# Kernel optimization log

Hardware: AMD Instinct MI355X
Metric: run time of the kernel (lower is better)

## Reference

```python
import jax, jax.numpy as jnp
import numpy as np

H = 1024     # hidden_size
NH = 16      # num heads
HD = H // NH # head_dim = 64
I = 4096     # intermediate_size
EPS = 1e-6


def rmsnorm(x, w, eps=EPS):
    var = jnp.mean(jnp.square(x), axis=-1, keepdims=True)
    return x * jax.lax.rsqrt(var + eps) * w


def attention(x, ctx, wq, wk, wv, wo):
    # x: [B,S,H], ctx: [B,Skv,H]; weights stored [in,out]
    B, S, _ = x.shape
    Skv = ctx.shape[1]
    q = (x @ wq).reshape(B, S, NH, HD)
    k = (ctx @ wk).reshape(B, Skv, NH, HD)
    v = (ctx @ wv).reshape(B, Skv, NH, HD)
    scores = jnp.einsum('bqhd,bkhd->bhqk', q, k) * (HD ** -0.5)
    attn = jax.nn.softmax(scores.astype(jnp.float32), axis=-1).astype(q.dtype)
    out = jnp.einsum('bhqk,bkhd->bqhd', attn, v).reshape(B, S, NH * HD)
    return out @ wo


def mlp(x, wg, wu, wd):
    return (jax.nn.silu(x @ wg) * (x @ wu)) @ wd


def setup_inputs() -> dict:
    key = jax.random.key(0)
    ks = jax.random.split(key, 16)
    p = lambda k, shape: (jax.random.normal(k, shape, jnp.float32) * 0.02)
    return {
        'hidden_states': jax.random.normal(ks[0], (1, 2048, H), jnp.float32),
        'context': jax.random.normal(ks[1], (1, 2048, H), jnp.float32),
        'sa_norm_w': jnp.ones((H,), jnp.float32),
        'sa_wq': p(ks[2], (H, NH * HD)),
        'sa_wk': p(ks[3], (H, NH * HD)),
        'sa_wv': p(ks[4], (H, NH * HD)),
        'sa_wo': p(ks[5], (NH * HD, H)),
        'ca_norm_w': jnp.ones((H,), jnp.float32),
        'ca_wq': p(ks[6], (H, NH * HD)),
        'ca_wk': p(ks[7], (H, NH * HD)),
        'ca_wv': p(ks[8], (H, NH * HD)),
        'ca_wo': p(ks[9], (NH * HD, H)),
        'mlp_norm_w': jnp.ones((H,), jnp.float32),
        'w_gate': p(ks[10], (H, I)),
        'w_up': p(ks[11], (H, I)),
        'w_down': p(ks[12], (I, H)),
    }


def reference(hidden_states, context, sa_norm_w, sa_wq, sa_wk, sa_wv, sa_wo,
              ca_norm_w, ca_wq, ca_wk, ca_wv, ca_wo,
              mlp_norm_w, w_gate, w_up, w_down):
    # self-attention block
    residual = hidden_states
    h = rmsnorm(hidden_states, sa_norm_w)
    h = residual + attention(h, h, sa_wq, sa_wk, sa_wv, sa_wo)
    # cross-attention block
    residual = h
    hn = rmsnorm(h, ca_norm_w)
    h = residual + attention(hn, context, ca_wq, ca_wk, ca_wv, ca_wo)
    # MLP block
    residual = h
    hn = rmsnorm(h, mlp_norm_w)
    h = residual + mlp(hn, w_gate, w_up, w_down)
    return h
```

## Files before the change

### kernel.cpp

```cpp
#include <hip/hip_runtime.h>

#define H 1024
#define S 2048
#define NH 16
#define HD 64
#define ISZ 4096

typedef __attribute__((ext_vector_type(8))) short s8v;
typedef __attribute__((ext_vector_type(4))) short s4v;
typedef __attribute__((ext_vector_type(4))) float f4v;
typedef __attribute__((ext_vector_type(2))) unsigned u2v;

#define MFMA16 __builtin_amdgcn_mfma_f32_16x16x32_bf16

__device__ __forceinline__ short f2bf(float f) {
    unsigned u = __builtin_bit_cast(unsigned, f);
    unsigned r = (u + 0x7FFFu + ((u >> 16) & 1u)) >> 16;
    return (short)r;
}
__device__ __forceinline__ float bf2f(short s) {
    unsigned u = ((unsigned)(unsigned short)s) << 16;
    return __builtin_bit_cast(float, u);
}
__device__ __forceinline__ float exp2_hw(float x) {
    float r; asm("v_exp_f32 %0, %1" : "=v"(r) : "v"(x)); return r;
}
__device__ __forceinline__ unsigned cvt_pk_bf16(float lo, float hi) {
    unsigned r; asm("v_cvt_pk_bf16_f32 %0, %1, %2" : "=v"(r) : "v"(lo), "v"(hi)); return r;
}

__device__ __forceinline__ void gload_lds16(const short* g, short* l) {
    __builtin_amdgcn_global_load_lds(
        (const __attribute__((address_space(1))) void*)g,
        (__attribute__((address_space(3))) void*)l, 16, 0, 0);
}

template <int N> struct VMt { static constexpr int val = N; };

struct PreArgs {
    const void* hid; const void* ctx;
    const void* sanw; const void* canw; const void* mlpnw;
    const void* w[11];
    short* hidc; short* ctxc; short* xn;
    short* canw_o; short* mlpnw_o;
    short* wT[11];
    int* flag_out;
};

__device__ __forceinline__ void tr_tile(const void* src, short* dst, int K, int N,
                                        int k0, int n0, int rmul, int roff,
                                        int isbf, float* tile ) {
    int t = threadIdx.x;
    int c = t & 31, r0 = t >> 5;
    if (isbf) {
        const short* s = (const short*)src;
#pragma unroll
        for (int i = 0; i < 4; i++)
            tile[(r0 + i * 8) * 33 + c] = bf2f(s[(k0 + r0 + i * 8) * N + n0 + c]);
    } else {
        const float* s = (const float*)src;
#pragma unroll
        for (int i = 0; i < 4; i++)
            tile[(r0 + i * 8) * 33 + c] = s[(k0 + r0 + i * 8) * N + n0 + c];
    }
    __syncthreads();
#pragma unroll
    for (int i = 0; i < 4; i++)
        dst[((n0 + r0 + i * 8) * rmul + roff) * K + k0 + c] = f2bf(tile[c * 33 + r0 + i * 8]);
}

__global__ __launch_bounds__(256) void preamble_kernel(PreArgs pa) {
    __shared__ float tile[32 * 33];
    __shared__ float red[4];
    int b = blockIdx.x;
    int t = threadIdx.x;
    int isbf = (((const unsigned*)pa.sanw)[0] == 0x3F803F80u);
    if (blockIdx.x == 0 && t == 0) pa.flag_out[0] = isbf;

    if (b < 2048) {
        int row = b;
        float xf[4];
        if (isbf) {
            s4v xv = *(const s4v*)((const short*)pa.hid + row * H + t * 4);
#pragma unroll
            for (int j = 0; j < 4; j++) xf[j] = bf2f(xv[j]);
        } else {
            const float* s = (const float*)pa.hid + row * H + t * 4;
#pragma unroll
            for (int j = 0; j < 4; j++) xf[j] = s[j];
        }
        float ss = 0.f;
        s4v cv;
#pragma unroll
        for (int j = 0; j < 4; j++) { cv[j] = f2bf(xf[j]); xf[j] = bf2f(cv[j]); ss += xf[j] * xf[j]; }
        *(s4v*)(pa.hidc + row * H + t * 4) = cv;
        int lane = t & 63, wid = t >> 6;
#pragma unroll
        for (int off = 32; off >= 1; off >>= 1) ss += __shfl_xor(ss, off);
        if (lane == 0) red[wid] = ss;
        __syncthreads();
        float tot = red[0] + red[1] + red[2] + red[3];
        float scale = rsqrtf(tot * (1.f / (float)H) + 1e-6f);
        float wv[4];
        if (isbf) {
            s4v wq = *(const s4v*)((const short*)pa.sanw + t * 4);
#pragma unroll
            for (int j = 0; j < 4; j++) wv[j] = bf2f(wq[j]);
        } else {
            const float* s = (const float*)pa.sanw + t * 4;
#pragma unroll
            for (int j = 0; j < 4; j++) wv[j] = s[j];
        }
        s4v ov;
#pragma unroll
        for (int j = 0; j < 4; j++) ov[j] = f2bf(xf[j] * scale * wv[j]);
        *(s4v*)(pa.xn + row * H + t * 4) = ov;
        return;
    }
    b -= 2048;
    if (b < 1024) {
        int i8 = b * 2048 + t * 8;
        if (isbf) {
            *(s8v*)(pa.ctxc + i8) = *(const s8v*)((const short*)pa.ctx + i8);
        } else {
            const float* s = (const float*)pa.ctx;
            s8v o;
#pragma unroll
            for (int j = 0; j < 8; j++) o[j] = f2bf(s[i8 + j]);
            *(s8v*)(pa.ctxc + i8) = o;
        }
        return;
    }
    b -= 1024;
    if (b < 2) {
        const void* src = (b == 0) ? pa.canw : pa.mlpnw;
        short* dst = (b == 0) ? pa.canw_o : pa.mlpnw_o;
        if (isbf) { if (t * 4 < H) *(s4v*)(dst + t * 4) = *(const s4v*)((const short*)src + t * 4); }
        else {
            const float* s = (const float*)src;
            s4v o;
#pragma unroll
            for (int j = 0; j < 4; j++) o[j] = f2bf(s[t * 4 + j]);
            *(s4v*)(dst + t * 4) = o;
        }
        return;
    }
    b -= 2;
    if (b < 8 * 1024) {
        int w = b >> 10, tl = b & 1023;
        tr_tile(pa.w[w], pa.wT[w], H, H, (tl & 31) * 32, (tl >> 5) * 32, 1, 0, isbf, tile);
        return;
    }
    b -= 8 * 1024;
    if (b < 2 * 4096) {
        int w = 8 + (b >> 12), tl = b & 4095;
        tr_tile(pa.w[w], pa.wT[8], H, ISZ, (tl & 31) * 32, (tl >> 5) * 32, 2, w - 8, isbf, tile);
        return;
    }
    b -= 2 * 4096;
    {
        tr_tile(pa.w[10], pa.wT[10], ISZ, H, (b & 127) * 32, (b >> 7) * 32, 1, 0, isbf, tile);
    }
}

__global__ __launch_bounds__(256) void rmsnorm_kernel(const short* __restrict__ x,
                                                      const short* __restrict__ w,
                                                      short* __restrict__ out) {
    int row = blockIdx.x;
    int t = threadIdx.x;
    int lane = t & 63, wid = t >> 6;
    const short* xr = x + row * H;

    s4v xv = *(const s4v*)(xr + t * 4);
    float xf[4];
    float ss = 0.f;
#pragma unroll
    for (int j = 0; j < 4; j++) { xf[j] = bf2f(xv[j]); ss += xf[j] * xf[j]; }
#pragma unroll
    for (int off = 32; off >= 1; off >>= 1) ss += __shfl_xor(ss, off);

    __shared__ float red[4];
    if (lane == 0) red[wid] = ss;
    __syncthreads();
    float tot = red[0] + red[1] + red[2] + red[3];
    float scale = rsqrtf(tot * (1.f / (float)H) + 1e-6f);

    s4v wv = *(const s4v*)(w + t * 4);
    s4v ov;
#pragma unroll
    for (int j = 0; j < 4; j++) ov[j] = f2bf(xf[j] * scale * bf2f(wv[j]));
    *(s4v*)(out + row * H + t * 4) = ov;
}

template <int BM_, int BN_>
__global__ __launch_bounds__(512, 2) void gemm_bt_kernel(
    const short* __restrict__ A0, const short* __restrict__ A1, int split, int lda,
    const short* __restrict__ Bt,
    void* __restrict__ C, int ldc, int K,
    const short* __restrict__ res,
    const int* __restrict__ dtype_flag,
    short* __restrict__ vtbuf, int vcol0,
    short* __restrict__ silu_out) {

    constexpr int MC = BM_ / 32;
    constexpr int NC = BN_ / 64;
    constexpr int U  = (BM_ + BN_) / 8;
    constexpr int PT = U / 8;
    constexpr int BUF = (BM_ + BN_) * 64;

    __shared__ short lds[2 * BUF];

    const short* A = (blockIdx.y < split) ? A0 : A1;
    int m0 = blockIdx.x * BM_;
    int n0 = blockIdx.y * BN_;

    int t = threadIdx.x;
    int lane = t & 63, wid = t >> 6;
    int quad = lane >> 4, l15 = lane & 15;
    int wr = wid >> 2, wc = wid & 3;
    int ld4 = lane >> 2, lc8 = (lane & 3) * 8;

    f4v acc[MC][NC] = {};

    auto stage = [&](short* buf, int k0) {
#pragma unroll
        for (int s = 0; s < PT; ++s) {
            int u = wid * PT + s;
            if (u < BM_ / 8) {
                int h = u / (BM_ / 16), r16 = u % (BM_ / 16);
                gload_lds16(A + (m0 + r16 * 16 + ld4) * lda + k0 + h * 32 + lc8,
                            buf + h * (BM_ * 32) + r16 * 512);
            } else {
                int ub = u - BM_ / 8;
                int h = ub / (BN_ / 16), r16 = ub % (BN_ / 16);
                gload_lds16(Bt + (n0 + r16 * 16 + ld4) * K + k0 + h * 32 + lc8,
                            buf + BM_ * 64 + h * (BN_ * 32) + r16 * 512);
            }
        }
    };

    auto compute = [&](const short* buf) {
#pragma unroll
        for (int kh = 0; kh < 2; ++kh) {
            s8v af[MC], bfv[NC];
#pragma unroll
            for (int mc = 0; mc < MC; ++mc)
                af[mc] = *(const s8v*)(buf + kh * (BM_ * 32) +
                                       (wr * (BM_ / 2) + mc * 16 + l15) * 32 + quad * 8);
#pragma unroll
            for (int nc = 0; nc < NC; ++nc)
                bfv[nc] = *(const s8v*)(buf + BM_ * 64 + kh * (BN_ * 32) +
                                        (wc * (BN_ / 4) + nc * 16 + l15) * 32 + quad * 8);
#pragma unroll
            for (int mc = 0; mc < MC; ++mc)
#pragma unroll
                for (int nc = 0; nc < NC; ++nc)
                    acc[mc][nc] = MFMA16(af[mc], bfv[nc], acc[mc][nc], 0, 0, 0);
        }
    };

    const int KT = K / 64;
    stage(lds, 0);
    __syncthreads();
    int cur = 0;
    for (int kt = 0; kt < KT - 1; ++kt) {
        stage(lds + (cur ^ 1) * BUF, (kt + 1) * 64);
        compute(lds + cur * BUF);
        __syncthreads();
        cur ^= 1;
    }
    compute(lds + cur * BUF);

    if (silu_out) {
#pragma unroll
        for (int mc = 0; mc < MC; mc++) {
#pragma unroll
            for (int nc = 0; nc < NC; nc++) {
                int row = m0 + wr * (BM_ / 2) + mc * 16 + quad * 4;
                int col = n0 + wc * (BN_ / 4) + nc * 16 + l15;
#pragma unroll
                for (int r = 0; r < 4; r++) {
                    float v = acc[mc][nc][r];
                    float other = __shfl_xor(v, 1);
                    if ((l15 & 1) == 0) {
                        float sig = 1.f / (1.f + __expf(-v));
                        silu_out[(row + r) * ISZ + (col >> 1)] = f2bf(v * sig * other);
                    }
                }
            }
        }
        return;
    }

    int out_fp32 = (dtype_flag != nullptr) && (dtype_flag[0] == 0);

#pragma unroll
    for (int mc = 0; mc < MC; mc++) {
#pragma unroll
        for (int nc = 0; nc < NC; nc++) {
            int row = m0 + wr * (BM_ / 2) + mc * 16 + quad * 4;
            int col = n0 + wc * (BN_ / 4) + nc * 16 + l15;
#pragma unroll
            for (int r = 0; r < 4; r++) {
                float vf = acc[mc][nc][r];
                if (res) vf += bf2f(res[(row + r) * ldc + col]);
                if (vtbuf && col >= vcol0)
                    vtbuf[(col - vcol0) * S + row + r] = f2bf(vf);
                else if (out_fp32)
                    ((float*)C)[(row + r) * ldc + col] = vf;
                else
                    ((short*)C)[(row + r) * ldc + col] = f2bf(vf);
            }
        }
    }
}

template <int BM_, int BN_>
__global__ __launch_bounds__(512, 2) void gemm_np_kernel(
    const short* __restrict__ A, int lda,
    const short* __restrict__ Bt,
    void* __restrict__ C, int ldc, int K,
    const short* __restrict__ res,
    const int* __restrict__ dtype_flag) {

    constexpr int MC = BM_ / 32;
    constexpr int NC = BN_ / 64;
    constexpr int PT = (BM_ + BN_) / 64;
    constexpr int BUF = (BM_ + BN_) * 64;

    __shared__ short lds[4 * BUF];

    int lin = blockIdx.x;
    int sw = (lin & 7) * 32 + (lin >> 3);
    int m0 = (sw & 31) * BM_;
    int n0 = (sw >> 5) * BN_;

    int t_ = threadIdx.x;
    int lane = t_ & 63, wid = t_ >> 6;
    int quad = lane >> 4, l15 = lane & 15;
    int wr = wid >> 2, wc = wid & 3;
    int ld4 = lane >> 2;
    int lcs = (((lane & 3) ^ ((ld4 >> 1) & 3)) * 8);
    int sq  = quad ^ ((l15 >> 1) & 3);

    f4v acc[MC][NC] = {};

    auto stage = [&](int bi, int kt) {
        short* buf = lds + bi * BUF;
        int k0 = kt * 64;
#pragma unroll
        for (int s = 0; s < PT; ++s) {
            int u = wid * PT + s;
            if (u < BM_ / 8) {
                int hh = u / (BM_ / 16), r16 = u % (BM_ / 16);
                gload_lds16(A + (m0 + r16 * 16 + ld4) * lda + k0 + hh * 32 + lcs,
                            buf + hh * (BM_ * 32) + r16 * 512);
            } else {
                int ub = u - BM_ / 8;
                int hh = ub / (BN_ / 16), r16 = ub % (BN_ / 16);
                gload_lds16(Bt + (n0 + r16 * 16 + ld4) * K + k0 + hh * 32 + lcs,
                            buf + BM_ * 64 + hh * (BN_ * 32) + r16 * 512);
            }
        }
    };

    auto tile = [&](int t, auto wt) {
        constexpr int W = decltype(wt)::val;
        if constexpr (W == 9)      asm volatile("s_waitcnt vmcnt(9)" ::: "memory");
        else if constexpr (W == 6) asm volatile("s_waitcnt vmcnt(6)" ::: "memory");
        else if constexpr (W == 3) asm volatile("s_waitcnt vmcnt(3)" ::: "memory");
        else                       asm volatile("s_waitcnt vmcnt(0)" ::: "memory");
        __builtin_amdgcn_s_barrier();
        const short* bc = lds + (t & 3) * BUF;
        s8v af[2][MC], bv[2][NC];
#pragma unroll
        for (int kh = 0; kh < 2; ++kh) {
#pragma unroll
            for (int mc = 0; mc < MC; ++mc)
                af[kh][mc] = *(const s8v*)(bc + kh * (BM_ * 32) +
                                           (wr * (BM_ / 2) + mc * 16 + l15) * 32 + sq * 8);
#pragma unroll
            for (int nc = 0; nc < NC; ++nc)
                bv[kh][nc] = *(const s8v*)(bc + BM_ * 64 + kh * (BN_ * 32) +
                                           (wc * (BN_ / 4) + nc * 16 + l15) * 32 + sq * 8);
        }
        asm volatile("s_waitcnt lgkmcnt(0)" ::: "memory");
        __builtin_amdgcn_s_barrier();
        __builtin_amdgcn_s_setprio(1);
#pragma unroll
        for (int kh = 0; kh < 2; ++kh)
#pragma unroll
            for (int mc = 0; mc < MC; ++mc)
#pragma unroll
                for (int nc = 0; nc < NC; ++nc)
                    acc[mc][nc] = MFMA16(af[kh][mc], bv[kh][nc], acc[mc][nc], 0, 0, 0);
        __builtin_amdgcn_s_setprio(0);
    };

    const int KT = K / 64;
    stage(0, 0); stage(1, 1); stage(2, 2);
    for (int t = 0; t < KT - 3; ++t) {
        stage((t + 3) & 3, t + 3);
        tile(t, VMt<9>{});
    }
    tile(KT - 3, VMt<6>{});
    tile(KT - 2, VMt<3>{});
    tile(KT - 1, VMt<0>{});

    int out_fp32 = (dtype_flag != nullptr) && (dtype_flag[0] == 0);
#pragma unroll
    for (int mc = 0; mc < MC; mc++) {
#pragma unroll
        for (int nc = 0; nc < NC; nc++) {
            int row = m0 + wr * (BM_ / 2) + mc * 16 + quad * 4;
            int col = n0 + wc * (BN_ / 4) + nc * 16 + l15;
#pragma unroll
            for (int r = 0; r < 4; r++) {
                float vf = acc[mc][nc][r];
                if (res) vf += bf2f(res[(row + r) * ldc + col]);
                if (out_fp32)
                    ((float*)C)[(row + r) * ldc + col] = vf;
                else
                    ((short*)C)[(row + r) * ldc + col] = f2bf(vf);
            }
        }
    }
}

__global__ __launch_bounds__(512, 2) void gemm_gu8_kernel(
    const short* __restrict__ A, const short* __restrict__ Bt,
    short* __restrict__ silu_out) {

    __shared__ short lds[65536];

    int lin = blockIdx.x;
    int sw = (lin & 7) * 32 + (lin >> 3);
    int m0 = (sw & 7) * 256;
    int n0 = (sw >> 3) * 256;

    int t = threadIdx.x;
    int lane = t & 63, wid = t >> 6;
    int quad = lane >> 4, l15 = lane & 15;
    int wr = wid >> 2, wc = wid & 3;
    int ld4 = lane >> 2;
    int lcs = (((lane & 3) ^ ((ld4 >> 1) & 3)) * 8);
    int sq  = quad ^ ((l15 >> 1) & 3);

    f4v acc[8][4] = {};

    const short* Arow = A + (m0 + ld4) * 1024 + lcs;
    const short* Brow = Bt + (n0 + ld4) * 1024 + lcs;

    auto stA = [&](int buf, int kt, int kh) {
        short* d = lds + buf * 32768 + kh * 8192;
#pragma unroll
        for (int i = 0; i < 2; i++) {
            int r0 = (wid + 8 * i) * 16;
            gload_lds16(Arow + r0 * 1024 + kt * 64 + kh * 32, d + r0 * 32);
        }
    };
    auto stB = [&](int buf, int kt, int kh) {
        short* d = lds + buf * 32768 + 16384 + kh * 8192;
#pragma unroll
        for (int i = 0; i < 2; i++) {
            int r0 = (wid + 8 * i) * 16;
            gload_lds16(Brow + r0 * 1024 + kt * 64 + kh * 32, d + r0 * 32);
        }
    };

    const int aoff = (wr * 128 + l15) * 32 + sq * 8;
    const int boff = 16384 + (wc * 64 + l15) * 32 + sq * 8;

    stA(0, 0, 0); stB(0, 0, 0); stA(0, 0, 1); stB(0, 0, 1);
    asm volatile("s_waitcnt vmcnt(4)" ::: "memory");
    __builtin_amdgcn_s_barrier();

    int cur = 0;
    for (int kt = 0; kt < 15; ++kt) {
        const short* bc = lds + cur * 32768;
        int nb = cur ^ 1;
        s8v af[8], b0, b1;

#pragma unroll
        for (int mc = 0; mc < 8; ++mc) af[mc] = *(const s8v*)(bc + aoff + mc * 512);
        b0 = *(const s8v*)(bc + boff);
        b1 = *(const s8v*)(bc + boff + 512);
        stA(nb, kt + 1, 0);
        __builtin_amdgcn_s_barrier();
        asm volatile("s_waitcnt lgkmcnt(0)" ::: "memory");
        __builtin_amdgcn_s_setprio(1);
#pragma unroll
        for (int mc = 0; mc < 8; ++mc) {
            acc[mc][0] = MFMA16(af[mc], b0, acc[mc][0], 0, 0, 0);
            acc[mc][1] = MFMA16(af[mc], b1, acc[mc][1], 0, 0, 0);
        }
        __builtin_amdgcn_s_setprio(0);
        __builtin_amdgcn_s_barrier();

        b0 = *(const s8v*)(bc + boff + 1024);
        b1 = *(const s8v*)(bc + boff + 1536);
        stB(nb, kt + 1, 0);
        asm volatile("s_waitcnt vmcnt(4)" ::: "memory");
        __builtin_amdgcn_s_barrier();
        asm volatile("s_waitcnt lgkmcnt(0)" ::: "memory");
        __builtin_amdgcn_s_setprio(1);
#pragma unroll
        for (int mc = 0; mc < 8; ++mc) {
            acc[mc][2] = MFMA16(af[mc], b0, acc[mc][2], 0, 0, 0);
            acc[mc][3] = MFMA16(af[mc], b1, acc[mc][3], 0, 0, 0);
        }
        __builtin_amdgcn_s_setprio(0);
        __builtin_amdgcn_s_barrier();

#pragma unroll
        for (int mc = 0; mc < 8; ++mc) af[mc] = *(const s8v*)(bc + 8192 + aoff + mc * 512);
        b0 = *(const s8v*)(bc + 8192 + boff);
        b1 = *(const s8v*)(bc + 8192 + boff + 512);
        stA(nb, kt + 1, 1);
        __builtin_amdgcn_s_barrier();
        asm volatile("s_waitcnt lgkmcnt(0)" ::: "memory");
        __builtin_amdgcn_s_setprio(1);
#pragma unroll
        for (int mc = 0; mc < 8; ++mc) {
            acc[mc][0] = MFMA16(af[mc], b0, acc[mc][0], 0, 0, 0);
            acc[mc][1] = MFMA16(af[mc], b1, acc[mc][1], 0, 0, 0);
        }
        __builtin_amdgcn_s_setprio(0);
        __builtin_amdgcn_s_barrier();

        b0 = *(const s8v*)(bc + 8192 + boff + 1024);
        b1 = *(const s8v*)(bc + 8192 + boff + 1536);
        stB(nb, kt + 1, 1);
        asm volatile("s_waitcnt vmcnt(4)" ::: "memory");
        __builtin_amdgcn_s_barrier();
        asm volatile("s_waitcnt lgkmcnt(0)" ::: "memory");
        __builtin_amdgcn_s_setprio(1);
#pragma unroll
        for (int mc = 0; mc < 8; ++mc) {
            acc[mc][2] = MFMA16(af[mc], b0, acc[mc][2], 0, 0, 0);
            acc[mc][3] = MFMA16(af[mc], b1, acc[mc][3], 0, 0, 0);
        }
        __builtin_amdgcn_s_setprio(0);
        __builtin_amdgcn_s_barrier();

        cur ^= 1;
    }

    asm volatile("s_waitcnt vmcnt(0)" ::: "memory");
    __builtin_amdgcn_s_barrier();
    {
        const short* bc = lds + cur * 32768;
#pragma unroll
        for (int kh = 0; kh < 2; ++kh) {
            s8v af[8], bv[4];
#pragma unroll
            for (int mc = 0; mc < 8; ++mc) af[mc] = *(const s8v*)(bc + kh * 8192 + aoff + mc * 512);
#pragma unroll
            for (int nc = 0; nc < 4; ++nc) bv[nc] = *(const s8v*)(bc + kh * 8192 + boff + nc * 512);
#pragma unroll
            for (int mc = 0; mc < 8; ++mc)
#pragma unroll
                for (int nc = 0; nc < 4; ++nc)
                    acc[mc][nc] = MFMA16(af[mc], bv[nc], acc[mc][nc], 0, 0, 0);
        }
    }

#pragma unroll
    for (int mc = 0; mc < 8; mc++) {
#pragma unroll
        for (int nc = 0; nc < 4; nc++) {
            int row = m0 + wr * 128 + mc * 16 + quad * 4;
            int col = n0 + wc * 64 + nc * 16 + l15;
#pragma unroll
            for (int r = 0; r < 4; r++) {
                float v = acc[mc][nc][r];
                float other = __shfl_xor(v, 1);
                if ((l15 & 1) == 0) {
                    float sig = 1.f / (1.f + __expf(-v));
                    silu_out[(row + r) * ISZ + (col >> 1)] = f2bf(v * sig * other);
                }
            }
        }
    }
}

__global__ __launch_bounds__(512, 4) void flash_attn_kernel(const short* __restrict__ q,
                                                            const short* __restrict__ kk,
                                                            const short* __restrict__ vt,
                                                            int rs,
                                                            short* __restrict__ o) {
    __shared__ short lds[40960];

    int h = blockIdx.y;
    int q0 = blockIdx.x * 64;
    int t = threadIdx.x;
    int lane = t & 63, wid = t >> 6;
    int quad = lane >> 4, l15 = lane & 15;
    int gw = wid & 3, gh = wid >> 2;
    int kvbase = gh * 1024;
    int kro = l15 & 7;

    int lrow = lane >> 3;
    int lsrc = ((lane & 7) ^ lrow) * 8;

    auto stageKV = [&](int buf, int tt) {
        int kvt = kvbase + tt * 64;
        short* kb = lds + (gh * 2 + buf) * 4096;
        short* vb = lds + 16384 + (gh * 2 + buf) * 4096;
#pragma unroll
        for (int i = 0; i < 2; i++) {
            int r0 = gw * 16 + i * 8;
            gload_lds16(kk + (kvt + r0 + lrow) * rs + h * HD + lsrc, kb + r0 * 64);
            gload_lds16(vt + (h * HD + r0 + lrow) * S + kvt + lsrc, vb + r0 * 64);
        }
    };

    const float qscale = 0.125f * 1.44269504f;
    s8v bq[2];
    int qrow = q0 + gw * 16 + l15;
#pragma unroll
    for (int c = 0; c < 2; c++) {
        s8v raw = *(const s8v*)(q + qrow * rs + h * HD + c * 32 + quad * 8);
#pragma unroll
        for (int j = 0; j < 8; j++) bq[c][j] = f2bf(qscale * bf2f(raw[j]));
    }

    f4v o_acc[4] = {};
    float m_s = -INFINITY, l_s = 0.f;
    short* pw = lds + 32768 + wid * 1024;

    const int NT = 16;
    stageKV(0, 0);
    __syncthreads();
    int cur = 0;
    for (int tt = 0; tt < NT; ++tt) {
        if (tt + 1 < NT) stageKV(cur ^ 1, tt + 1);
        const short* kb = lds + (gh * 2 + cur) * 4096;
        const short* vb = lds + 16384 + (gh * 2 + cur) * 4096;

        f4v st[4];
#pragma unroll
        for (int kc = 0; kc < 4; kc++) {
            f4v a_ = (f4v){0.f, 0.f, 0.f, 0.f};
#pragma unroll
            for (int dc = 0; dc < 2; dc++) {
                s8v kf = *(const s8v*)(kb + (kc * 16 + l15) * 64 + ((dc * 4 + quad) ^ kro) * 8);
                a_ = MFMA16(kf, bq[dc], a_, 0, 0, 0);
            }
            st[kc] = a_;
        }

        float mloc = -INFINITY;
#pragma unroll
        for (int kc = 0; kc < 4; kc++)
#pragma unroll
            for (int r = 0; r < 4; r++) mloc = fmaxf(mloc, st[kc][r]);
        mloc = fmaxf(mloc, __shfl_xor(mloc, 16));
        mloc = fmaxf(mloc, __shfl_xor(mloc, 32));
        float m_new = fmaxf(m_s, mloc);
        float alpha = exp2_hw(m_s - m_new);
        float lloc = 0.f;
#pragma unroll
        for (int kc = 0; kc < 4; kc++)
#pragma unroll
            for (int r = 0; r < 4; r++) {
                float p = exp2_hw(st[kc][r] - m_new);
                st[kc][r] = p;
                lloc += p;
            }
        lloc += __shfl_xor(lloc, 16);
        lloc += __shfl_xor(lloc, 32);
        l_s = l_s * alpha + lloc;
        m_s = m_new;
#pragma unroll
        for (int nd = 0; nd < 4; nd++)
#pragma unroll
            for (int r = 0; r < 4; r++) o_acc[nd][r] *= alpha;

#pragma unroll
        for (int kc = 0; kc < 4; kc++) {
            u2v w;
            w[0] = cvt_pk_bf16(st[kc][0], st[kc][1]);
            w[1] = cvt_pk_bf16(st[kc][2], st[kc][3]);
            int pslot = (kc * 2 + (quad >> 1)) ^ kro;
            *(u2v*)(pw + l15 * 64 + pslot * 8 + (quad & 1) * 4) = w;
        }

#pragma unroll
        for (int nd = 0; nd < 4; nd++) {
#pragma unroll
            for (int kc2 = 0; kc2 < 2; kc2++) {
                s8v vf = *(const s8v*)(vb + (nd * 16 + l15) * 64 + ((kc2 * 4 + quad) ^ kro) * 8);
                s8v pf = *(const s8v*)(pw + l15 * 64 + ((kc2 * 4 + quad) ^ kro) * 8);
                o_acc[nd] = MFMA16(vf, pf, o_acc[nd], 0, 0, 0);
            }
        }
        __syncthreads();
        cur ^= 1;
    }

    float* ex = (float*)lds;
    if (gh == 1) {
        int base = (gw * 64 + lane) * 20;
#pragma unroll
        for (int nd = 0; nd < 4; nd++) *(f4v*)(ex + base + nd * 4) = o_acc[nd];
        ex[base + 16] = m_s;
        ex[base + 17] = l_s;
    }
    __syncthreads();
    if (gh == 1) return;

    int base = (wid * 64 + lane) * 20;
    float mB = ex[base + 16], lB = ex[base + 17];
    float M = fmaxf(m_s, mB);
    float a = exp2_hw(m_s - M), bsc = exp2_hw(mB - M);
    float inv = 1.f / (a * l_s + bsc * lB);
#pragma unroll
    for (int nd = 0; nd < 4; nd++) {
        f4v ob = *(const f4v*)(ex + base + nd * 4);
#pragma unroll
        for (int r = 0; r < 4; r++)
            o_acc[nd][r] = (a * o_acc[nd][r] + bsc * ob[r]) * inv;
    }

#pragma unroll
    for (int nd = 0; nd < 4; nd++)
#pragma unroll
        for (int r = 0; r < 4; r++)
            pw[l15 * 64 + nd * 16 + quad * 4 + r] = f2bf(o_acc[nd][r]);

    int qr = lane >> 2, dc2 = (lane & 3) * 16;
    s8v x0 = *(const s8v*)(pw + qr * 64 + dc2);
    s8v x1 = *(const s8v*)(pw + qr * 64 + dc2 + 8);
    short* dst = o + (q0 + wid * 16 + qr) * H + h * HD + dc2;
    *(s8v*)(dst) = x0;
    *(s8v*)(dst + 8) = x1;
}

extern "C" void kernel_launch(void* const* d_in, const int* in_sizes, int n_in,
                              void* d_out, int out_size, void* d_ws, size_t ws_size,
                              hipStream_t stream) {
    const int SH = S * H;
    const int WH = H * H;
    const int WI = H * ISZ;

    int* flag = (int*)d_ws;
    short* base = (short*)d_ws + 16;

    short* hidc   = base;
    short* ctxc   = hidc + SH;
    short* sanw   = ctxc + SH;
    short* canw   = sanw + H;
    short* mlpnw  = canw + H;
    short* saqkvT = mlpnw + H;
    short* sawoT  = saqkvT + 3 * WH;
    short* caqkvT = sawoT + WH;
    short* cawoT  = caqkvT + 3 * WH;
    short* wguT   = cawoT + WH;
    short* wdT    = wguT + 2 * WI;
    short* xn     = wdT + WI;
    short* qkv    = xn + SH;
    short* ao     = qkv + 3 * SH;
    short* h1     = ao + SH;
    short* gu     = qkv;
    short* h2     = qkv + 8 * SH;
    short* vt     = h2 + SH;

    dim3 blk(256);
    dim3 blk2(512);

    PreArgs pa;
    pa.hid = d_in[0]; pa.ctx = d_in[1];
    pa.sanw = d_in[2]; pa.canw = d_in[7]; pa.mlpnw = d_in[12];
    const void* wsrc[11] = {d_in[3], d_in[4], d_in[5], d_in[6],
                            d_in[8], d_in[9], d_in[10], d_in[11],
                            d_in[13], d_in[14], d_in[15]};
    short* wdst[11] = {saqkvT, saqkvT + WH, saqkvT + 2 * WH, sawoT,
                       caqkvT, caqkvT + WH, caqkvT + 2 * WH, cawoT,
                       wguT, wguT , wdT};
    for (int i = 0; i < 11; i++) { pa.w[i] = wsrc[i]; pa.wT[i] = wdst[i]; }
    pa.hidc = hidc; pa.ctxc = ctxc; pa.xn = xn;
    pa.canw_o = canw; pa.mlpnw_o = mlpnw;
    pa.flag_out = flag;
    const int pre_blocks = 2048 + 1024 + 2 + 8 * 1024 + 2 * 4096 + 4096;
    preamble_kernel<<<pre_blocks, blk, 0, stream>>>(pa);

    gemm_bt_kernel<128, 128><<<dim3(S / 128, 3 * H / 128), blk2, 0, stream>>>(
        xn, xn, 24, H, saqkvT, qkv, 3 * H, H, nullptr, nullptr, vt, 2 * H, nullptr);
    flash_attn_kernel<<<dim3(S / 64, NH), blk2, 0, stream>>>(qkv, qkv + H, vt, 3 * H, ao);
    gemm_np_kernel<64, 128><<<dim3(256), blk2, 0, stream>>>(
        ao, H, sawoT, h1, H, H, hidc, nullptr);

    rmsnorm_kernel<<<S, blk, 0, stream>>>(h1, canw, xn);
    gemm_bt_kernel<128, 128><<<dim3(S / 128, 3 * H / 128), blk2, 0, stream>>>(
        xn, ctxc, 8, H, caqkvT, qkv, 3 * H, H, nullptr, nullptr, vt, 2 * H, nullptr);
    flash_attn_kernel<<<dim3(S / 64, NH), blk2, 0, stream>>>(qkv, qkv + H, vt, 3 * H, ao);
    gemm_np_kernel<64, 128><<<dim3(256), blk2, 0, stream>>>(
        ao, H, cawoT, h2, H, H, h1, nullptr);

    rmsnorm_kernel<<<S, blk, 0, stream>>>(h2, mlpnw, xn);
    gemm_gu8_kernel<<<dim3(256), blk2, 0, stream>>>(xn, wguT, gu);
    gemm_np_kernel<64, 128><<<dim3(256), blk2, 0, stream>>>(
        gu, ISZ, wdT, d_out, H, ISZ, h2, flag);
}
```

Before: 424.5 us.

## Deepen gate/up GEMM pipeline to 4-slot ring with 3 tiles in flight

Restructures the fused gate/up GEMM main loop from double-buffered 64-wide K tiles to a 4-deep ring of 32-wide K tiles. Three tiles are prefetched ahead, with vmcnt waits tuned per tail iteration. The goal is to hide global-to-LDS load latency better. It also removes the XOR swizzle on LDS addressing, which may introduce bank conflicts on the fragment reads.

```diff
diff --git a/kernel.cpp b/kernel.cpp
--- a/kernel.cpp
+++ b/kernel.cpp
@@ -442,50 +442,48 @@
     int lane = t & 63, wid = t >> 6;
     int quad = lane >> 4, l15 = lane & 15;
     int wr = wid >> 2, wc = wid & 3;
-    int ld4 = lane >> 2;
-    int lcs = (((lane & 3) ^ ((ld4 >> 1) & 3)) * 8);
-    int sq  = quad ^ ((l15 >> 1) & 3);
+    int ld4 = lane >> 2, lc8 = (lane & 3) * 8;
 
     f4v acc[8][4] = {};
 
-    const short* Arow = A + (m0 + ld4) * 1024 + lcs;
-    const short* Brow = Bt + (n0 + ld4) * 1024 + lcs;
-
-    auto stA = [&](int buf, int kt, int kh) {
-        short* d = lds + buf * 32768 + kh * 8192;
+    const short* Arow = A + (m0 + ld4) * 1024 + lc8;
+    const short* Brow = Bt + (n0 + ld4) * 1024 + lc8;
+
+    auto stA = [&](int buf, int kt) {
+        short* d = lds + buf * 16384;
 #pragma unroll
         for (int i = 0; i < 2; i++) {
             int r0 = (wid + 8 * i) * 16;
-            gload_lds16(Arow + r0 * 1024 + kt * 64 + kh * 32, d + r0 * 32);
+            gload_lds16(Arow + r0 * 1024 + kt * 32, d + r0 * 32);
         }
     };
-    auto stB = [&](int buf, int kt, int kh) {
-        short* d = lds + buf * 32768 + 16384 + kh * 8192;
+    auto stB = [&](int buf, int kt) {
+        short* d = lds + buf * 16384 + 8192;
 #pragma unroll
         for (int i = 0; i < 2; i++) {
             int r0 = (wid + 8 * i) * 16;
-            gload_lds16(Brow + r0 * 1024 + kt * 64 + kh * 32, d + r0 * 32);
+            gload_lds16(Brow + r0 * 1024 + kt * 32, d + r0 * 32);
         }
     };
 
-    const int aoff = (wr * 128 + l15) * 32 + sq * 8;
-    const int boff = 16384 + (wc * 64 + l15) * 32 + sq * 8;
-
-    stA(0, 0, 0); stB(0, 0, 0); stA(0, 0, 1); stB(0, 0, 1);
-    asm volatile("s_waitcnt vmcnt(4)" ::: "memory");
+    const int aoff = (wr * 128 + l15) * 32 + quad * 8;
+    const int boff = 8192 + (wc * 64 + l15) * 32 + quad * 8;
+
+    stA(0, 0); stB(0, 0);
+    stA(1, 1); stB(1, 1);
+    stA(2, 2); stB(2, 2);
+    asm volatile("s_waitcnt vmcnt(8)" ::: "memory");
     __builtin_amdgcn_s_barrier();
 
-    int cur = 0;
-    for (int kt = 0; kt < 15; ++kt) {
-        const short* bc = lds + cur * 32768;
-        int nb = cur ^ 1;
+    auto ktile = [&](int kt, bool do_stage, auto wt) {
+        constexpr int W = decltype(wt)::val;
+        const short* bc = lds + (kt & 3) * 16384;
         s8v af[8], b0, b1;
-
 #pragma unroll
         for (int mc = 0; mc < 8; ++mc) af[mc] = *(const s8v*)(bc + aoff + mc * 512);
         b0 = *(const s8v*)(bc + boff);
         b1 = *(const s8v*)(bc + boff + 512);
-        stA(nb, kt + 1, 0);
+        if (do_stage) stA((kt + 3) & 3, kt + 3);
         __builtin_amdgcn_s_barrier();
         asm volatile("s_waitcnt lgkmcnt(0)" ::: "memory");
         __builtin_amdgcn_s_setprio(1);
@@ -496,11 +494,12 @@
         }
         __builtin_amdgcn_s_setprio(0);
         __builtin_amdgcn_s_barrier();
-
         b0 = *(const s8v*)(bc + boff + 1024);
         b1 = *(const s8v*)(bc + boff + 1536);
-        stB(nb, kt + 1, 0);
-        asm volatile("s_waitcnt vmcnt(4)" ::: "memory");
+        if (do_stage) stB((kt + 3) & 3, kt + 3);
+        if constexpr (W == 8)      asm volatile("s_waitcnt vmcnt(8)" ::: "memory");
+        else if constexpr (W == 4) asm volatile("s_waitcnt vmcnt(4)" ::: "memory");
+        else if constexpr (W == 0) asm volatile("s_waitcnt vmcnt(0)" ::: "memory");
         __builtin_amdgcn_s_barrier();
         asm volatile("s_waitcnt lgkmcnt(0)" ::: "memory");
         __builtin_amdgcn_s_setprio(1);
@@ -511,59 +510,12 @@
         }
         __builtin_amdgcn_s_setprio(0);
         __builtin_amdgcn_s_barrier();
-
-#pragma unroll
-        for (int mc = 0; mc < 8; ++mc) af[mc] = *(const s8v*)(bc + 8192 + aoff + mc * 512);
-        b0 = *(const s8v*)(bc + 8192 + boff);
-        b1 = *(const s8v*)(bc + 8192 + boff + 512);
-        stA(nb, kt + 1, 1);
-        __builtin_amdgcn_s_barrier();
-        asm volatile("s_waitcnt lgkmcnt(0)" ::: "memory");
-        __builtin_amdgcn_s_setprio(1);
-#pragma unroll
-        for (int mc = 0; mc < 8; ++mc) {
-            acc[mc][0] = MFMA16(af[mc], b0, acc[mc][0], 0, 0, 0);
-            acc[mc][1] = MFMA16(af[mc], b1, acc[mc][1], 0, 0, 0);
-        }
-        __builtin_amdgcn_s_setprio(0);
-        __builtin_amdgcn_s_barrier();
-
-        b0 = *(const s8v*)(bc + 8192 + boff + 1024);
-        b1 = *(const s8v*)(bc + 8192 + boff + 1536);
-        stB(nb, kt + 1, 1);
-        asm volatile("s_waitcnt vmcnt(4)" ::: "memory");
-        __builtin_amdgcn_s_barrier();
-        asm volatile("s_waitcnt lgkmcnt(0)" ::: "memory");
-        __builtin_amdgcn_s_setprio(1);
-#pragma unroll
-        for (int mc = 0; mc < 8; ++mc) {
-            acc[mc][2] = MFMA16(af[mc], b0, acc[mc][2], 0, 0, 0);
-            acc[mc][3] = MFMA16(af[mc], b1, acc[mc][3], 0, 0, 0);
-        }
-        __builtin_amdgcn_s_setprio(0);
-        __builtin_amdgcn_s_barrier();
-
-        cur ^= 1;
-    }
-
-    asm volatile("s_waitcnt vmcnt(0)" ::: "memory");
-    __builtin_amdgcn_s_barrier();
-    {
-        const short* bc = lds + cur * 32768;
-#pragma unroll
-        for (int kh = 0; kh < 2; ++kh) {
-            s8v af[8], bv[4];
-#pragma unroll
-            for (int mc = 0; mc < 8; ++mc) af[mc] = *(const s8v*)(bc + kh * 8192 + aoff + mc * 512);
-#pragma unroll
-            for (int nc = 0; nc < 4; ++nc) bv[nc] = *(const s8v*)(bc + kh * 8192 + boff + nc * 512);
-#pragma unroll
-            for (int mc = 0; mc < 8; ++mc)
-#pragma unroll
-                for (int nc = 0; nc < 4; ++nc)
-                    acc[mc][nc] = MFMA16(af[mc], bv[nc], acc[mc][nc], 0, 0, 0);
-        }
-    }
+    };
+
+    for (int kt = 0; kt < 29; ++kt) ktile(kt, true, VMt<8>{});
+    ktile(29, false, VMt<4>{});
+    ktile(30, false, VMt<0>{});
+    ktile(31, false, VMt<-1>{});
 
 #pragma unroll
     for (int mc = 0; mc < 8; mc++) {
```

New measurement: 425.5 us. About the same (+0.2%).
